# Kernel tuning notes

Measured on AMD Instinct MI355X. Metric: run time of the kernel, lower is better.

## Reference

```python
import jax, jax.numpy as jnp
import numpy as np

LP, LQ, B, D0, H = 128, 128, 64, 150, 150
D = 2 * D0  # in_size after self-concatenation


def setup_inputs() -> dict:
    key = jax.random.key(0)
    ks = jax.random.split(key, 12)
    s = 0.08  # weight scale to keep tanh/sigmoid out of hard saturation
    return {
        "Up": jax.random.normal(ks[0], (LP, B, D0), jnp.float32),
        "Uq": jax.random.normal(ks[1], (LQ, B, D0), jnp.float32),
        "Wp": jax.random.normal(ks[2], (H, D), jnp.float32) * s,
        "Wq": jax.random.normal(ks[3], (H, D), jnp.float32) * s,
        "Wv": jax.random.normal(ks[4], (H, H), jnp.float32) * s,
        "Wg": jax.random.normal(ks[5], (2 * D, 2 * D), jnp.float32) * s,
        "V": jax.random.normal(ks[6], (B, H), jnp.float32) * s,
        "v0": jax.random.normal(ks[7], (B, H), jnp.float32) * s,
        "W_ih": jax.random.normal(ks[8], (3 * H, 2 * D), jnp.float32) * s,
        "W_hh": jax.random.normal(ks[9], (3 * H, H), jnp.float32) * s,
        "b_ih": jax.random.normal(ks[10], (3 * H,), jnp.float32) * s,
        "b_hh": jax.random.normal(ks[11], (3 * H,), jnp.float32) * s,
    }


def reference(Up, Uq, Wp, Wq, Wv, Wg, V, v0, W_ih, W_hh, b_ih, b_hh):
    # self-concat of features, as in the original forward
    Upc = jnp.concatenate([Up, Up], axis=2)  # (LP, B, D)
    Uqc = jnp.concatenate([Uq, Uq], axis=2)  # (LQ, B, D)
    # Wq @ Uq is loop-invariant in the original; hoist it (same math)
    Wuq = jnp.einsum('lbd,hd->lbh', Uqc, Wq)  # (LQ, B, H)

    def step(v, up_i):
        # up_i: (B, D); v: (B, H)
        wup = up_i @ Wp.T                                   # (B, H)
        x = jnp.tanh(wup[None] + Wuq + (v @ Wv.T)[None])    # (LQ, B, H)
        s = jnp.einsum('lbh,bh->bl', x, V)                  # (B, LQ)
        a = jax.nn.softmax(s, axis=1)
        c = jnp.einsum('bl,lbd->bd', a, Uqc)                # (B, D)
        r = jnp.concatenate([up_i, c], axis=1)              # (B, 2D)
        r = jax.nn.sigmoid(r @ Wg.T) * r                    # gated input
        # PyTorch GRUCell math
        gi = r @ W_ih.T + b_ih                              # (B, 3H)
        gh = v @ W_hh.T + b_hh                              # (B, 3H)
        i_r, i_z, i_n = jnp.split(gi, 3, axis=1)
        h_r, h_z, h_n = jnp.split(gh, 3, axis=1)
        rr = jax.nn.sigmoid(i_r + h_r)
        zz = jax.nn.sigmoid(i_z + h_z)
        n = jnp.tanh(i_n + rr * h_n)
        h = (1.0 - zz) * n + zz * v
        return h, h

    _, vs = jax.lax.scan(step, v0, Upc)  # vs: (LP, B, H)
    return vs  # dropout in eval mode = identity
```

## Files before the change

kernel.cpp:

```cpp
#include <hip/hip_runtime.h>
#include <hip/hip_fp16.h>

typedef _Float16 h2_t __attribute__((ext_vector_type(2)));

__device__ __forceinline__ float dot2f(int w, int x, float acc) {
#if __has_builtin(__builtin_amdgcn_fdot2)
  return __builtin_amdgcn_fdot2(__builtin_bit_cast(h2_t, w),
                                __builtin_bit_cast(h2_t, x), acc, false);
#else
  h2_t a = __builtin_bit_cast(h2_t, w);
  h2_t b = __builtin_bit_cast(h2_t, x);
  return acc + (float)a[0] * (float)b[0] + (float)a[1] * (float)b[1];
#endif
}

__device__ __forceinline__ float rcp_f(float x) {
#if __has_builtin(__builtin_amdgcn_rcpf)
  return __builtin_amdgcn_rcpf(x);
#else
  return 1.0f / x;
#endif
}

__device__ __forceinline__ float fast_tanh(float x) {
  float e = exp2f(x * 2.885390082f);
  return 1.0f - 2.0f * rcp_f(e + 1.0f);
}
__device__ __forceinline__ float fast_sigmoid(float x) {
  return rcp_f(1.0f + exp2f(x * -1.442695041f));
}
__device__ __forceinline__ int packh2(float a, float b) {
  h2_t h;
  h[0] = (_Float16)a;
  h[1] = (_Float16)b;
  return __builtin_bit_cast(int, h);
}

__device__ __forceinline__ int ldi_coh(const int* p) {
  return __hip_atomic_load((int*)p, __ATOMIC_RELAXED, __HIP_MEMORY_SCOPE_AGENT);
}
__device__ __forceinline__ float ldf_coh(const float* p) {
  return __hip_atomic_load((float*)p, __ATOMIC_RELAXED,
                           __HIP_MEMORY_SCOPE_AGENT);
}
__device__ __forceinline__ void sti_coh(int* p, int v) {
  __hip_atomic_store(p, v, __ATOMIC_RELAXED, __HIP_MEMORY_SCOPE_AGENT);
}
__device__ __forceinline__ void stf_coh(float* p, float v) {
  __hip_atomic_store(p, v, __ATOMIC_RELAXED, __HIP_MEMORY_SCOPE_AGENT);
}

#define DOTC(W, X, A)                                                          \
  {                                                                            \
    int4 _x = (X);                                                             \
    A = dot2f((W).x, _x.x, A);                                                 \
    A = dot2f((W).y, _x.y, A);                                                 \
    A = dot2f((W).z, _x.z, A);                                                 \
    A = dot2f((W).w, _x.w, A);                                                 \
  }

__global__ void prep_weights(const float* __restrict__ Wp,
                             const float* __restrict__ Wv,
                             const float* __restrict__ Wg,
                             const float* __restrict__ Wih,
                             const float* __restrict__ Whh,
                             __half* __restrict__ oMa, __half* __restrict__ oWg,
                             __half* __restrict__ oWih,
                             __half* __restrict__ oWhh, int* __restrict__ flags,
                             int* __restrict__ payload) {
  if (blockIdx.x == 0) {
    for (int j = threadIdx.x; j < 1024; j += 256) flags[j] = 0;
  }
  if (blockIdx.x == 1 && threadIdx.x < 128) {
    int cc = threadIdx.x >> 1, s = threadIdx.x & 1;
    payload[cc * 4096 + 150 + s] = 0;
  }
  int idx = blockIdx.x * 256 + threadIdx.x;
  const int NMa = 150 * 304, NWg = 600 * 304, NWih = 900 * 304,
            NWhh = 452 * 152;
  if (idx < NMa) {
    int r = idx / 304, c = idx % 304;
    float v = 0.f;
    if (c < 150)
      v = Wp[r * 300 + c] + Wp[r * 300 + 150 + c];
    else if (c >= 152 && c < 302)
      v = Wv[r * 150 + (c - 152)];
    oMa[(c >> 3) * 1200 + r * 8 + (c & 7)] = __float2half(v);
    return;
  }
  idx -= NMa;
  if (idx < NWg) {
    int r = idx / 304, c = idx % 304;
    float v = 0.f;
    if (c < 150)
      v = Wg[r * 600 + c] + Wg[r * 600 + 150 + c];
    else if (c >= 152 && c < 302) {
      int d = c - 152;
      v = Wg[r * 600 + 300 + d] + Wg[r * 600 + 450 + d];
    }
    oWg[(c >> 3) * 4800 + r * 8 + (c & 7)] = __float2half(v);
    return;
  }
  idx -= NWg;
  if (idx < NWih) {
    int s = idx / 304, c = idx % 304;
    int r = s >> 1, off = (s & 1) * 300;
    float v = (c < 300) ? Wih[r * 600 + off + c] : 0.f;
    oWih[(c >> 3) * 7200 + s * 8 + (c & 7)] = __float2half(v);
    return;
  }
  idx -= NWih;
  if (idx < NWhh) {
    int r = idx / 152, c = idx % 152;
    float v = (r < 450 && c < 150) ? Whh[r * 150 + c] : 0.f;
    oWhh[(c >> 3) * 3616 + r * 8 + (c & 7)] = __float2half(v);
  }
}

__global__ __launch_bounds__(256) void prep_wuq(const float* __restrict__ Uq,
                                                const float* __restrict__ Wq,
                                                __half* __restrict__ oWuq,
                                                __half* __restrict__ oUqh) {
  __shared__ float sUql[64 * 150];
  const int l = blockIdx.x, tid = threadIdx.x;
  for (int idx = tid; idx < 9600; idx += 256) sUql[idx] = Uq[l * 9600 + idx];
  __syncthreads();
  for (int idx = tid; idx < 64 * 152; idx += 256) {
    int bb = idx / 152, d = idx % 152;
    float v = (d < 150) ? sUql[bb * 150 + d] : 0.f;
    oUqh[(size_t)bb * 19456 + l * 152 + d] = __float2half(v);
  }
  if (tid < 152) {
    const int h = tid;
    if (h < 150) {
      float wq[150];
#pragma unroll
      for (int d = 0; d < 150; ++d)
        wq[d] = Wq[h * 300 + d] + Wq[h * 300 + 150 + d];
      for (int bb = 0; bb < 64; ++bb) {
        float acc = 0.f;
#pragma unroll
        for (int d = 0; d < 150; ++d) acc += wq[d] * sUql[bb * 150 + d];
        oWuq[(size_t)bb * 19456 + l * 152 + h] = __float2half(acc);
      }
    } else {
      for (int bb = 0; bb < 64; ++bb)
        oWuq[(size_t)bb * 19456 + l * 152 + h] = __float2half(0.f);
    }
  }
}

__device__ __forceinline__ void post_and_wait(int* f4, int q, int target) {
  __syncthreads();
  if (threadIdx.x == 0) sti_coh(&f4[q], target);
  if (threadIdx.x < 4) {
    int spins = 0;
    while (ldi_coh(&f4[threadIdx.x]) < target && ++spins < (1 << 20)) {
    }
  }
  __syncthreads();
}

__global__ __launch_bounds__(1024, 1) void pq_main(
    const float* __restrict__ Up, const float* __restrict__ V,
    const float* __restrict__ v0, const float* __restrict__ b_ih,
    const float* __restrict__ b_hh, const int* __restrict__ gWuq,
    const __half* __restrict__ gUqh, const int* __restrict__ gMa,
    const int* __restrict__ gWg, const int* __restrict__ gWih,
    const int* __restrict__ gWhh, int* __restrict__ flags,
    int* __restrict__ payload, float* __restrict__ out) {
  __shared__ __align__(16) float sTV[304];
  __shared__ __align__(16) float sV[152];
  __shared__ __align__(16) float sGh[456];
  __shared__ __align__(16) float sS[128];
  __shared__ __align__(16) float sC0[152];
  __shared__ __align__(16) float sCp[608];
  __shared__ __align__(16) float sU[152];
  __shared__ __align__(16) float sv_[152];
  __shared__ __align__(16) int sXd[152];
  __shared__ __align__(16) int svh[76];
  __shared__ __align__(16) int sRgh[304];
  __shared__ __align__(16) float sGi[456];
  __shared__ __align__(16) float sBih[456];
  __shared__ __align__(16) float sBhh[456];
  extern __shared__ __align__(16) int dynlds[];
  int* sWuq = dynlds;
  __half* sUqh = (__half*)(dynlds + 9728);

  const int t = threadIdx.x;
  const int c = blockIdx.x & 63;
  const int q = blockIdx.x >> 6;
  const int b = c;

  int* myflags = flags + c * 16;
  int* pl = payload + c * 4096;
  float* plT = (float*)pl;
  float* plGh = (float*)(pl + 160);
  float* plGi = (float*)(pl + 640);

  const int4* MaT4 = (const int4*)gMa;
  const int4* WgT4 = (const int4*)gWg;
  const int4* WihT4 = (const int4*)gWih;
  const int4* WhhT4 = (const int4*)gWhh;

  const int baseR = 113 * q - (q == 3 ? 1 : 0);
  const int cntR = (q < 2) ? 113 : 112;
  const int c_lo = (q == 0) ? 0 : (q == 1) ? 18 : (q == 2) ? 38 : 56;
  const int c_hi = (q == 0) ? 18 : (q == 1) ? 37 : (q == 2) ? 56 : 75;

  int4 a0, a1, a2, a3, a4, a5, a6, a7, a8, a9;
  int4 b0, b1, b2, b3, b4, b5, b6, b7, b8, b9;
  {
    const int4* p;
    int nr, sub, step, nch, row;
    if (t < 152) {
      p = MaT4; nr = 150; step = 4; nch = 38;
      sub = t & 3; row = 38 * q + (t >> 2);
      if (row > 149) row = 149;
    } else if (t < 378) {
      p = WhhT4; nr = 452; step = 2; nch = 19;
      int u2 = t - 152; sub = u2 & 1; row = baseR + (u2 >> 1);
    } else if (t >= 384 && t < 984) {
      p = WgT4; nr = 600; step = 4; nch = 38;
      int u2 = t - 384; sub = u2 & 3; row = 150 * q + (u2 >> 2);
    } else {
      p = MaT4; nr = 150; step = 4; nch = 38; sub = 0; row = 0;
    }
#define LDA(i)                                                                 \
  {                                                                            \
    int cc = sub + step * (i);                                                 \
    if (cc > nch - 1) cc = nch - 1;                                            \
    a##i = p[cc * nr + row];                                                   \
  }
    LDA(0) LDA(1) LDA(2) LDA(3) LDA(4) LDA(5) LDA(6) LDA(7) LDA(8) LDA(9)
#undef LDA
  }
  {
    int row = (t < 900) ? (t >> 1) : 0;
    int sub = (t < 900) ? (t & 1) : 0;
#define LDB(i)                                                                 \
  {                                                                            \
    int cq = c_lo + sub + 2 * (i);                                             \
    if (cq > c_hi) cq = c_hi;                                                  \
    int hf = (cq >= 38) ? 1 : 0;                                               \
    int cc = cq - 38 * hf;                                                     \
    b##i = WihT4[cc * 900 + 2 * row + hf];                                     \
  }
    LDB(0) LDB(1) LDB(2) LDB(3) LDB(4) LDB(5) LDB(6) LDB(7) LDB(8) LDB(9)
#undef LDB
  }

  for (int idx = t; idx < 9728; idx += 1024) sWuq[idx] = gWuq[b * 9728 + idx];
  {
    const int* gU2 = (const int*)(gUqh + (size_t)b * 19456);
    int* sU2 = (int*)sUqh;
    for (int idx = t; idx < 9728; idx += 1024) sU2[idx] = gU2[idx];
  }
  if (t < 150) {
    sV[t] = V[b * 150 + t];
    float v_ = v0[b * 150 + t];
    sv_[t] = v_;
    float vn = __shfl_down(v_, 1);
    if (!(t & 1)) svh[t >> 1] = packh2(v_, vn);
    float u_ = Up[b * 150 + t];
    sU[t] = u_;
    float un = __shfl_down(u_, 1);
    if (!(t & 1)) sXd[t >> 1] = packh2(u_, un);
  }
  for (int idx = t; idx < 450; idx += 1024) {
    sBih[idx] = b_ih[idx];
    sBhh[idx] = b_hh[idx];
  }
  if (t < 304) sRgh[t] = 0;
  if (t == 0) {
    svh[75] = 0;
    sXd[75] = 0;
    sXd[151] = 0;
    sV[150] = 0.f;
    sV[151] = 0.f;
  }
  const int4* sXd4 = (const int4*)sXd;
  const int4* svh4 = (const int4*)svh;
  const int4* sRgh4 = (const int4*)sRgh;
  const int c_lq = t / 150;
  const int c_d0 = t - c_lq * 150;
  __syncthreads();

#pragma unroll 1
  for (int i = 0; i < 128; ++i) {
    float accD0 = 0.f, accD1 = 0.f;
    float unext = 0.f;
    if (t >= 640 && t < 790) {
      int ii = (i < 127) ? (i + 1) : 127;
      unext = Up[ii * 9600 + b * 150 + (t - 640)];
    }

    if (t < 152) {
      int rl = t >> 2, sub = t & 3;
      int h = 38 * q + rl;
      float acc0 = 0.f, acc1 = 0.f;
#define MAD(i2, A)                                                             \
  {                                                                            \
    int cc = sub + 4 * (i2);                                                   \
    if (cc < 38) {                                                             \
      int4 x = (cc < 19) ? sXd4[cc] : svh4[cc - 19];                           \
      DOTC(a##i2, x, A)                                                        \
    }                                                                          \
  }
      MAD(0, acc0) MAD(1, acc1) MAD(2, acc0) MAD(3, acc1) MAD(4, acc0)
      MAD(5, acc1) MAD(6, acc0) MAD(7, acc1) MAD(8, acc0) MAD(9, acc1)
#undef MAD
      float acc = acc0 + acc1;
      acc += __shfl_xor(acc, 1);
      acc += __shfl_xor(acc, 2);
      if (sub == 0 && h < 150) stf_coh(&plT[h], acc);
    } else if (t < 378) {
      int u2 = t - 152;
      int rl = u2 >> 1, sub = u2 & 1;
      int r = baseR + rl;
      float acc0 = 0.f, acc1 = 0.f;
#define HHD(i2, A)                                                             \
  {                                                                            \
    int cc = sub + 2 * (i2);                                                   \
    if (cc < 19) DOTC(a##i2, svh4[cc], A)                                      \
  }
      HHD(0, acc0) HHD(1, acc1) HHD(2, acc0) HHD(3, acc1) HHD(4, acc0)
      HHD(5, acc1) HHD(6, acc0) HHD(7, acc1) HHD(8, acc0) HHD(9, acc1)
#undef HHD
      float acc = acc0 + acc1;
      acc += __shfl_xor(acc, 1);
      if (sub == 0 && rl < cntR) stf_coh(&plGh[r], acc + sBhh[r]);
    } else if (t >= 384 && t < 984) {
      int sub = (t - 384) & 3;
#define WGU(i2, A)                                                             \
  {                                                                            \
    int cc = sub + 4 * (i2);                                                   \
    if (cc < 19) DOTC(a##i2, sXd4[cc], A)                                      \
  }
      WGU(0, accD0) WGU(1, accD1) WGU(2, accD0) WGU(3, accD1) WGU(4, accD0)
#undef WGU
    }
    post_and_wait(myflags, q, i + 1);
    if (t < 76) {
      float x0 = ldf_coh(&plT[2 * t]);
      float x1 = ldf_coh(&plT[2 * t + 1]);
      float4 tv;
      tv.x = x0;
      tv.y = x1;
      tv.z = sV[2 * t];
      tv.w = sV[2 * t + 1];
      ((float4*)sTV)[t] = tv;
    } else if (t >= 128 && t < 578) {
      sGh[t - 128] = ldf_coh(&plGh[t - 128]);
    }
    __syncthreads();

    {
      const int l = t >> 3, sub = t & 7;
      const int base = l * 76;
      const int niter = (sub < 3) ? 10 : 9;
      float acc = 0.f;
#pragma unroll
      for (int k = 0; k < 10; ++k) {
        if (k < niter) {
          int w = sub + 8 * k;
          int qq = sWuq[base + w];
          float4 tv = ((const float4*)sTV)[w];
          h2_t hq = __builtin_bit_cast(h2_t, qq);
          float x0 = (float)hq[0] + tv.x;
          float x1 = (float)hq[1] + tv.y;
          acc += fast_tanh(x0) * tv.z;
          acc += fast_tanh(x1) * tv.w;
        }
      }
      acc += __shfl_xor(acc, 1);
      acc += __shfl_xor(acc, 2);
      acc += __shfl_xor(acc, 4);
      if (sub == 0) sS[l] = acc;
    }
    __syncthreads();

    if (t < 64) {
      float s0 = sS[t], s1 = sS[t + 64];
      float m = fmaxf(s0, s1);
#pragma unroll
      for (int o = 1; o < 64; o <<= 1) m = fmaxf(m, __shfl_xor(m, o));
      float e0 = exp2f((s0 - m) * 1.442695041f);
      float e1 = exp2f((s1 - m) * 1.442695041f);
      float sum = e0 + e1;
#pragma unroll
      for (int o = 1; o < 64; o <<= 1) sum += __shfl_xor(sum, o);
      float inv = rcp_f(sum);
      sS[t] = e0 * inv;
      sS[t + 64] = e1 * inv;
    }
    __syncthreads();

    if (t < 600) {
      const __half* src = sUqh + c_lq * 32 * 152 + c_d0;
      float acc = 0.f;
#pragma unroll
      for (int j = 0; j < 32; ++j) {
        float a = sS[c_lq * 32 + j];
        acc += a * __half2float(src[j * 152]);
      }
      sCp[c_lq * 152 + c_d0] = acc;
    }
    __syncthreads();
    if (t < 150) {
      float c0 = sCp[t] + sCp[152 + t] + sCp[304 + t] + sCp[456 + t];
      sC0[t] = c0;
      float cn = __shfl_down(c0, 1);
      if (!(t & 1)) sXd[76 + (t >> 1)] = packh2(c0, cn);
    }
    __syncthreads();

    if (t >= 384 && t < 984) {
      int u2 = t - 384;
      int rl = u2 >> 2, sub = u2 & 3;
      int j = 150 * q + rl;
#define WGC(i2, A)                                                             \
  {                                                                            \
    int cc = sub + 4 * (i2);                                                   \
    if (cc >= 19 && cc < 38) DOTC(a##i2, sXd4[cc], A)                          \
  }
      WGC(4, accD1) WGC(5, accD0) WGC(6, accD1) WGC(7, accD0) WGC(8, accD1)
      WGC(9, accD0)
#undef WGC
      float acc = accD0 + accD1;
      acc += __shfl_xor(acc, 1);
      acc += __shfl_xor(acc, 2);
      if (sub == 0) {
        float rb;
        if (j < 150)
          rb = sU[j];
        else if (j < 300)
          rb = sU[j - 150];
        else if (j < 450)
          rb = sC0[j - 300];
        else
          rb = sC0[j - 450];
        float rg = rb * fast_sigmoid(acc);
        ((__half*)sRgh)[(j < 300) ? j : (j + 4)] = __float2half(rg);
      }
    }
    __syncthreads();

    if (t < 900) {
      int row = t >> 1, sub = t & 1;
      float acc0 = 0.f, acc1 = 0.f;
#define IHD(i2, A)                                                             \
  {                                                                            \
    int cq = c_lo + sub + 2 * (i2);                                            \
    if (cq <= c_hi) DOTC(b##i2, sRgh4[cq], A)                                  \
  }
      IHD(0, acc0) IHD(1, acc1) IHD(2, acc0) IHD(3, acc1) IHD(4, acc0)
      IHD(5, acc1) IHD(6, acc0) IHD(7, acc1) IHD(8, acc0) IHD(9, acc1)
#undef IHD
      float acc = acc0 + acc1;
      acc += __shfl_xor(acc, 1);
      if (!sub) stf_coh(&plGi[456 * q + row], acc);
    }
    post_and_wait(myflags + 4, q, i + 1);
    if (t < 450) {
      float g0 = ldf_coh(&plGi[t]);
      float g1 = ldf_coh(&plGi[456 + t]);
      float g2 = ldf_coh(&plGi[912 + t]);
      float g3 = ldf_coh(&plGi[1368 + t]);
      sGi[t] = g0 + g1 + g2 + g3 + sBih[t];
    }
    __syncthreads();

    if (t < 150) {
      float ir = sGi[t], iz = sGi[150 + t], in_ = sGi[300 + t];
      float hr = sGh[t], hz = sGh[150 + t], hn = sGh[300 + t];
      float rr = fast_sigmoid(ir + hr);
      float zz = fast_sigmoid(iz + hz);
      float nn = fast_tanh(in_ + rr * hn);
      float vold = sv_[t];
      float hv = nn + zz * (vold - nn);
      if (q == 0) out[i * 9600 + b * 150 + t] = hv;
      sv_[t] = hv;
      float hv1 = __shfl_down(hv, 1);
      if (!(t & 1)) svh[t >> 1] = packh2(hv, hv1);
    } else if (t >= 640 && t < 790) {
      int t2 = t - 640;
      sU[t2] = unext;
      float un = __shfl_down(unext, 1);
      if (!(t2 & 1)) sXd[t2 >> 1] = packh2(unext, un);
    }
    __syncthreads();
  }
}

extern "C" void kernel_launch(void* const* d_in, const int* in_sizes, int n_in,
                              void* d_out, int out_size, void* d_ws,
                              size_t ws_size, hipStream_t stream) {
  const float* Up = (const float*)d_in[0];
  const float* Uq = (const float*)d_in[1];
  const float* Wp = (const float*)d_in[2];
  const float* Wq = (const float*)d_in[3];
  const float* Wv = (const float*)d_in[4];
  const float* Wg = (const float*)d_in[5];
  const float* V = (const float*)d_in[6];
  const float* v0 = (const float*)d_in[7];
  const float* Wih = (const float*)d_in[8];
  const float* Whh = (const float*)d_in[9];
  const float* bih = (const float*)d_in[10];
  const float* bhh = (const float*)d_in[11];

  char* ws = (char*)d_ws;
  __half* wsWuq = (__half*)(ws);
  __half* wsUqh = (__half*)(ws + 2490368);
  __half* wsMa = (__half*)(ws + 4980736);
  __half* wsWg = (__half*)(ws + 5071936);
  __half* wsWih = (__half*)(ws + 5436736);
  __half* wsWhh = (__half*)(ws + 5983936);
  int* wsFlags = (int*)(ws + 6121472);
  int* wsPayload = (int*)(ws + 6125568);

  (void)hipFuncSetAttribute((const void*)pq_main,
                            hipFuncAttributeMaxDynamicSharedMemorySize, 77824);

  prep_weights<<<2228, 256, 0, stream>>>(Wp, Wv, Wg, Wih, Whh, wsMa, wsWg,
                                         wsWih, wsWhh, wsFlags, wsPayload);
  prep_wuq<<<128, 256, 0, stream>>>(Uq, Wq, wsWuq, wsUqh);
  pq_main<<<256, 1024, 77824, stream>>>(Up, V, v0, bih, bhh, (const int*)wsWuq,
                                        wsUqh, (const int*)wsMa,
                                        (const int*)wsWg, (const int*)wsWih,
                                        (const int*)wsWhh, wsFlags, wsPayload,
                                        (float*)d_out);
}
```

Before: 1.441 ms.

## Split attention score by hidden slice per block, exchange partial scores instead of projections

Each of the four cooperating blocks now keeps its own slice of the Wp/Wv projection in LDS and computes partial attention scores over its 38 hidden units. Only the partial scores are exchanged through the coherent payload, where the four slices are summed. The separate max-subtracted softmax pass is replaced by an unnormalized exp, with the 1/sum folded into the context vector. The spin-wait gets s_sleep, and the Wg dot product is computed in one pass after the context instead of being split around the barrier. This removes one LDS-to-global round trip of projections and a barrier stage, but drops the max subtraction, which risks overflow for large scores, and it moves the Up-half of the Wg work back onto the critical path.

```diff
diff --git a/kernel.cpp b/kernel.cpp
--- a/kernel.cpp
+++ b/kernel.cpp
@@ -70,10 +70,6 @@
                              int* __restrict__ payload) {
   if (blockIdx.x == 0) {
     for (int j = threadIdx.x; j < 1024; j += 256) flags[j] = 0;
-  }
-  if (blockIdx.x == 1 && threadIdx.x < 128) {
-    int cc = threadIdx.x >> 1, s = threadIdx.x & 1;
-    payload[cc * 4096 + 150 + s] = 0;
   }
   int idx = blockIdx.x * 256 + threadIdx.x;
   const int NMa = 150 * 304, NWg = 600 * 304, NWih = 900 * 304,
@@ -156,6 +152,7 @@
   if (threadIdx.x < 4) {
     int spins = 0;
     while (ldi_coh(&f4[threadIdx.x]) < target && ++spins < (1 << 20)) {
+      __builtin_amdgcn_s_sleep(1);
     }
   }
   __syncthreads();
@@ -173,6 +170,7 @@
   __shared__ __align__(16) float sV[152];
   __shared__ __align__(16) float sGh[456];
   __shared__ __align__(16) float sS[128];
+  __shared__ __align__(16) float sSS[4];
   __shared__ __align__(16) float sC0[152];
   __shared__ __align__(16) float sCp[608];
   __shared__ __align__(16) float sU[152];
@@ -194,9 +192,9 @@
 
   int* myflags = flags + c * 16;
   int* pl = payload + c * 4096;
-  float* plT = (float*)pl;
-  float* plGh = (float*)(pl + 160);
-  float* plGi = (float*)(pl + 640);
+  float* plS = (float*)pl;
+  float* plGh = (float*)(pl + 512);
+  float* plGi = (float*)(pl + 1024);
 
   const int4* MaT4 = (const int4*)gMa;
   const int4* WgT4 = (const int4*)gWg;
@@ -271,7 +269,10 @@
     sBih[idx] = b_ih[idx];
     sBhh[idx] = b_hh[idx];
   }
-  if (t < 304) sRgh[t] = 0;
+  if (t < 304) {
+    sRgh[t] = 0;
+    sTV[t] = 0.f;
+  }
   if (t == 0) {
     svh[75] = 0;
     sXd[75] = 0;
@@ -288,7 +289,6 @@
 
 #pragma unroll 1
   for (int i = 0; i < 128; ++i) {
-    float accD0 = 0.f, accD1 = 0.f;
     float unext = 0.f;
     if (t >= 640 && t < 790) {
       int ii = (i < 127) ? (i + 1) : 127;
@@ -297,7 +297,6 @@
 
     if (t < 152) {
       int rl = t >> 2, sub = t & 3;
-      int h = 38 * q + rl;
       float acc0 = 0.f, acc1 = 0.f;
 #define MAD(i2, A)                                                             \
   {                                                                            \
@@ -313,7 +312,17 @@
       float acc = acc0 + acc1;
       acc += __shfl_xor(acc, 1);
       acc += __shfl_xor(acc, 2);
-      if (sub == 0 && h < 150) stf_coh(&plT[h], acc);
+      float accN = __shfl_down(acc, 4);
+      if (sub == 0 && !(rl & 1)) {
+        int w = 19 * q + (rl >> 1);
+        int h = 38 * q + rl;
+        float4 tv;
+        tv.x = acc;
+        tv.y = accN;
+        tv.z = sV[h];
+        tv.w = sV[h + 1];
+        ((float4*)sTV)[w] = tv;
+      }
     } else if (t < 378) {
       int u2 = t - 152;
       int rl = u2 >> 1, sub = u2 & 1;
@@ -330,40 +339,18 @@
       float acc = acc0 + acc1;
       acc += __shfl_xor(acc, 1);
       if (sub == 0 && rl < cntR) stf_coh(&plGh[r], acc + sBhh[r]);
-    } else if (t >= 384 && t < 984) {
-      int sub = (t - 384) & 3;
-#define WGU(i2, A)                                                             \
-  {                                                                            \
-    int cc = sub + 4 * (i2);                                                   \
-    if (cc < 19) DOTC(a##i2, sXd4[cc], A)                                      \
-  }
-      WGU(0, accD0) WGU(1, accD1) WGU(2, accD0) WGU(3, accD1) WGU(4, accD0)
-#undef WGU
-    }
-    post_and_wait(myflags, q, i + 1);
-    if (t < 76) {
-      float x0 = ldf_coh(&plT[2 * t]);
-      float x1 = ldf_coh(&plT[2 * t + 1]);
-      float4 tv;
-      tv.x = x0;
-      tv.y = x1;
-      tv.z = sV[2 * t];
-      tv.w = sV[2 * t + 1];
-      ((float4*)sTV)[t] = tv;
-    } else if (t >= 128 && t < 578) {
-      sGh[t - 128] = ldf_coh(&plGh[t - 128]);
     }
     __syncthreads();
 
     {
       const int l = t >> 3, sub = t & 7;
       const int base = l * 76;
-      const int niter = (sub < 3) ? 10 : 9;
       float acc = 0.f;
 #pragma unroll
-      for (int k = 0; k < 10; ++k) {
-        if (k < niter) {
-          int w = sub + 8 * k;
+      for (int k = 0; k < 3; ++k) {
+        int wl = sub + 8 * k;
+        if (wl < 19) {
+          int w = 19 * q + wl;
           int qq = sWuq[base + w];
           float4 tv = ((const float4*)sTV)[w];
           h2_t hq = __builtin_bit_cast(h2_t, qq);
@@ -376,23 +363,15 @@
       acc += __shfl_xor(acc, 1);
       acc += __shfl_xor(acc, 2);
       acc += __shfl_xor(acc, 4);
-      if (sub == 0) sS[l] = acc;
-    }
-    __syncthreads();
-
-    if (t < 64) {
-      float s0 = sS[t], s1 = sS[t + 64];
-      float m = fmaxf(s0, s1);
-#pragma unroll
-      for (int o = 1; o < 64; o <<= 1) m = fmaxf(m, __shfl_xor(m, o));
-      float e0 = exp2f((s0 - m) * 1.442695041f);
-      float e1 = exp2f((s1 - m) * 1.442695041f);
-      float sum = e0 + e1;
-#pragma unroll
-      for (int o = 1; o < 64; o <<= 1) sum += __shfl_xor(sum, o);
-      float inv = rcp_f(sum);
-      sS[t] = e0 * inv;
-      sS[t + 64] = e1 * inv;
+      if (sub == 0) stf_coh(&plS[128 * q + l], acc);
+    }
+    post_and_wait(myflags, q, i + 1);
+    if (t < 128) {
+      float s = ldf_coh(&plS[t]) + ldf_coh(&plS[128 + t]) +
+                ldf_coh(&plS[256 + t]) + ldf_coh(&plS[384 + t]);
+      sS[t] = exp2f(s * 1.442695041f);
+    } else if (t >= 128 && t < 578) {
+      sGh[t - 128] = ldf_coh(&plGh[t - 128]);
     }
     __syncthreads();
 
@@ -405,10 +384,17 @@
         acc += a * __half2float(src[j * 152]);
       }
       sCp[c_lq * 152 + c_d0] = acc;
+    } else if (t >= 960) {
+      int lane = t - 960;
+      float e = sS[lane] + sS[64 + lane];
+#pragma unroll
+      for (int o = 1; o < 64; o <<= 1) e += __shfl_xor(e, o);
+      if (lane == 0) sSS[0] = e;
     }
     __syncthreads();
     if (t < 150) {
-      float c0 = sCp[t] + sCp[152 + t] + sCp[304 + t] + sCp[456 + t];
+      float inv = rcp_f(sSS[0]);
+      float c0 = (sCp[t] + sCp[152 + t] + sCp[304 + t] + sCp[456 + t]) * inv;
       sC0[t] = c0;
       float cn = __shfl_down(c0, 1);
       if (!(t & 1)) sXd[76 + (t >> 1)] = packh2(c0, cn);
@@ -419,15 +405,16 @@
       int u2 = t - 384;
       int rl = u2 >> 2, sub = u2 & 3;
       int j = 150 * q + rl;
-#define WGC(i2, A)                                                             \
+      float acc0 = 0.f, acc1 = 0.f;
+#define WGD(i2, A)                                                             \
   {                                                                            \
     int cc = sub + 4 * (i2);                                                   \
-    if (cc >= 19 && cc < 38) DOTC(a##i2, sXd4[cc], A)                          \
-  }
-      WGC(4, accD1) WGC(5, accD0) WGC(6, accD1) WGC(7, accD0) WGC(8, accD1)
-      WGC(9, accD0)
-#undef WGC
-      float acc = accD0 + accD1;
+    if (cc < 38) DOTC(a##i2, sXd4[cc], A)                                      \
+  }
+      WGD(0, acc0) WGD(1, acc1) WGD(2, acc0) WGD(3, acc1) WGD(4, acc0)
+      WGD(5, acc1) WGD(6, acc0) WGD(7, acc1) WGD(8, acc0) WGD(9, acc1)
+#undef WGD
+      float acc = acc0 + acc1;
       acc += __shfl_xor(acc, 1);
       acc += __shfl_xor(acc, 2);
       if (sub == 0) {
```

Measured after the change: 1.233 ms. 1.17x faster.
